# Kernel optimization log

Hardware: AMD Instinct MI355X
Metric: run time of the kernel (lower is better)

Reference implementation:

```python
import jax, jax.numpy as jnp
import numpy as np

NUM_CLASS = 4096
HIDDEN = 512
N_GROUPS = 64  # per branch (co and cl)
BATCH = 64


def _make_group_of(rng, n_groups, num_class):
    # Ragged partition of [0, num_class) into n_groups contiguous segments,
    # mirroring len_co_list_index offsets of the original module.
    cuts = np.sort(rng.choice(np.arange(1, num_class), size=n_groups - 1, replace=False))
    sizes = np.diff(np.concatenate([[0], cuts, [num_class]]))
    return np.repeat(np.arange(n_groups), sizes)  # [num_class] -> group id per class slot


def setup_inputs() -> dict:
    key = jax.random.key(0)
    k_x, k_cow, k_clw, k_cob, k_clb = jax.random.split(key, 5)
    rng = np.random.default_rng(0)
    stdv = 1.0 / np.sqrt(HIDDEN)  # matches reset_parameters uniform(-stdv, stdv)

    x = jax.random.normal(k_x, (BATCH, 2 * N_GROUPS, HIDDEN), dtype=jnp.float32)
    co_W = jax.random.uniform(k_cow, (1, NUM_CLASS, HIDDEN), jnp.float32, -stdv, stdv)
    cl_W = jax.random.uniform(k_clw, (1, NUM_CLASS, HIDDEN), jnp.float32, -stdv, stdv)
    co_b = jax.random.uniform(k_cob, (1, NUM_CLASS), jnp.float32, -stdv, stdv)
    cl_b = jax.random.uniform(k_clb, (1, NUM_CLASS), jnp.float32, -stdv, stdv)

    co_group_of = jnp.asarray(_make_group_of(rng, N_GROUPS, NUM_CLASS), jnp.int32)
    cl_group_of = jnp.asarray(_make_group_of(rng, N_GROUPS, NUM_CLASS), jnp.int32)
    # co_index / cl_index are class-id permutations applied after concat
    co_index = jnp.asarray(rng.permutation(NUM_CLASS), jnp.int32)
    cl_index = jnp.asarray(rng.permutation(NUM_CLASS), jnp.int32)

    return {
        "x": x,
        "co_W": co_W, "cl_W": cl_W,
        "co_b": co_b, "cl_b": cl_b,
        "co_group_of": co_group_of, "cl_group_of": cl_group_of,
        "co_index": co_index, "cl_index": cl_index,
        "group_len": N_GROUPS,
    }


def reference(x, co_W, cl_W, co_b, cl_b, co_group_of, cl_group_of, co_index, cl_index, group_len):
    # x: [B, 2*G, H]; first G group-features feed the co branch, rest the cl branch.
    co_x = x[:, :group_len, :]   # [B, G, H]
    cl_x = x[:, group_len:, :]   # [B, G, H]

    # Fused ragged group-wise broadcast-multiply + reduce:
    # out[b, c] = dot(W[0, c], x[b, group_of[c]]) + b[0, c]
    co_out = jnp.einsum("bch,ch->bc", co_x[:, co_group_of, :], co_W[0]) + co_b  # [B, C]
    cl_out = jnp.einsum("bch,ch->bc", cl_x[:, cl_group_of, :], cl_W[0]) + cl_b  # [B, C]

    # Final index_select gather over classes
    return co_out[:, co_index], cl_out[:, cl_index]
```

## Files before the change

### kernel.cpp

```cpp
#include <hip/hip_runtime.h>
#include <hip/hip_bf16.h>
#include <string.h>

#define NUM_CLASS 4096
#define HIDDEN    512
#define NGROUPS   64
#define BATCH     64

#define WS_NWORK 0
#define WS_WORK  16
#define WS_INV   10240
#define TMP_OFF_F 16384
#define TMP_H_STRIDE (4096*64)
#define TMP_S_STRIDE (2*4096*64)

typedef __attribute__((ext_vector_type(8))) short short8;
typedef __attribute__((ext_vector_type(4))) float f32x4;

__device__ __forceinline__ unsigned int pack2bf(float a, float b) {
    __hip_bfloat16 ha = __float2bfloat16(a), hb = __float2bfloat16(b);
    unsigned short ua, ub;
    memcpy(&ua, &ha, 2); memcpy(&ub, &hb, 2);
    return (unsigned int)ua | ((unsigned int)ub << 16);
}

template<bool WITH_INV>
__global__ __launch_bounds__(1024) void prep_kernel(
    const int* __restrict__ co_gof, const int* __restrict__ cl_gof,
    const int* __restrict__ co_idx, const int* __restrict__ cl_idx,
    int* __restrict__ ws)
{
    __shared__ int s_starts[2][65];
    int tid = threadIdx.x;
    for (int v = tid; v < 2 * NUM_CLASS; v += 1024) {
        int h = v >> 12, c = v & (NUM_CLASS - 1);
        const int* gof = h ? cl_gof : co_gof;
        int g = gof[c];
        if (c == 0) { s_starts[h][0] = 0; s_starts[h][64] = NUM_CLASS; }
        else if (g != gof[c - 1]) s_starts[h][g] = c;
        if (WITH_INV) {
            const int* idx = h ? cl_idx : co_idx;
            ws[WS_INV + h * NUM_CLASS + idx[c]] = c;
        }
    }
    __syncthreads();
    if (tid < 64) {
        int lane = tid;
        for (int h = 0; h < 2; ++h) {
            int s = s_starts[h][lane], e = s_starts[h][lane + 1];
            int cnt = (e - s + 63) >> 6;
            int inc = cnt;
            #pragma unroll
            for (int d = 1; d < 64; d <<= 1) {
                int o = __shfl_up(inc, d, 64);
                if (lane >= d) inc += o;
            }
            int excl = inc - cnt;
            for (int t = 0; t < cnt; ++t) {
                int c0 = s + t * 64;
                int ncls = min(64, e - c0);
                ws[WS_WORK + h * 128 + excl + t] = (lane << 20) | (ncls << 12) | c0;
            }
            if (lane == 63) ws[WS_NWORK + h] = inc;
        }
    }
}

template<int KS, bool SCATTER>
__global__ __launch_bounds__(256, 4) void gwl_stage1(
    const float* __restrict__ x,
    const float* __restrict__ co_W, const float* __restrict__ cl_W,
    const float* __restrict__ co_b, const float* __restrict__ cl_b,
    int* __restrict__ ws, float* __restrict__ out)
{
    const int nblk = 128 * 2 * KS;
    const int chunk = nblk >> 3;
    int bid = blockIdx.x;
    int swz = (bid & 7) * chunk + (bid >> 3);
    int widx = swz & 127;
    int hk   = swz >> 7;
    int h    = hk & 1;
    int kh   = hk >> 1;

    int nw = ws[WS_NWORK + h];
    if (widx >= nw) return;
    int packed = ws[WS_WORK + h * 128 + widx];
    int c0 = packed & 0xFFF, ncls = (packed >> 12) & 0xFF, g = packed >> 20;
    const float* Wp = h ? cl_W : co_W;
    int xrow = h * 64 + g;

    __shared__ __align__(16) unsigned char smem[2][18432];

    int tid = threadIdx.x;
    int l = tid & 63, w = tid >> 6;

    int rowq[4], kvq[4], wcl[4];
    #pragma unroll
    for (int q = 0; q < 4; ++q) {
        int v = q * 256 + tid;
        rowq[q] = v >> 4;
        kvq[q]  = v & 15;
        wcl[q]  = min(rowq[q], ncls - 1);
    }

    float4 rxA[4], rwA[4], rxB[4], rwB[4];
    f32x4 acc[4];
    #pragma unroll
    for (int i = 0; i < 4; ++i) acc[i] = (f32x4)(0.0f);

    const int NCH = 8 / KS;
    const int kbase = kh * (HIDDEN / KS);

#define LOADC(T, RX, RW) do {                                                       \
    int k0_ = kbase + (T) * 64;                                                     \
    _Pragma("unroll")                                                               \
    for (int q = 0; q < 4; ++q) {                                                   \
        RX[q] = *(const float4*)(x + rowq[q] * 65536 + xrow * 512 + k0_ + kvq[q]*4);\
        RW[q] = *(const float4*)(Wp + (c0 + wcl[q]) * 512 + k0_ + kvq[q] * 4);      \
    } } while (0)

#define STOREC(BUF, RX, RW) do {                                                    \
    unsigned short (*Xs_)[72]  = (unsigned short(*)[72])smem[BUF];                  \
    unsigned short (*Wls_)[72] = (unsigned short(*)[72])(smem[BUF] + 9216);         \
    _Pragma("unroll")                                                               \
    for (int q = 0; q < 4; ++q) {                                                   \
        unsigned int x0 = pack2bf(RX[q].x, RX[q].y);                                \
        unsigned int x1 = pack2bf(RX[q].z, RX[q].w);                                \
        unsigned int w0 = pack2bf(RW[q].x, RW[q].y);                                \
        unsigned int w1 = pack2bf(RW[q].z, RW[q].w);                                \
        *(uint2*)&Xs_[rowq[q]][kvq[q] * 4]  = make_uint2(x0, x1);                   \
        *(uint2*)&Wls_[rowq[q]][kvq[q] * 4] = make_uint2(w0, w1);                   \
    } } while (0)

#define COMPUTEC(BUF) do {                                                          \
    unsigned short (*Xs_)[72]  = (unsigned short(*)[72])smem[BUF];                  \
    unsigned short (*Wls_)[72] = (unsigned short(*)[72])(smem[BUF] + 9216);         \
    _Pragma("unroll")                                                               \
    for (int kq = 0; kq < 2; ++kq) {                                                \
        int koff = kq * 32 + (l >> 4) * 8;                                          \
        short8 bfrag = *(const short8*)&Wls_[w * 16 + (l & 15)][koff];              \
        _Pragma("unroll")                                                           \
        for (int i = 0; i < 4; ++i) {                                               \
            short8 afrag = *(const short8*)&Xs_[16 * i + (l & 15)][koff];           \
            acc[i] = __builtin_amdgcn_mfma_f32_16x16x32_bf16(afrag, bfrag, acc[i],  \
                                                             0, 0, 0);              \
        }                                                                           \
    } } while (0)

    LOADC(0, rxA, rwA);
    if (NCH > 1) LOADC(1, rxB, rwB);
    STOREC(0, rxA, rwA);
    __syncthreads();
    #pragma unroll
    for (int t = 0; t < NCH; ++t) {
        if (t + 2 < NCH) {
            if (t & 1) LOADC(t + 2, rxB, rwB);
            else       LOADC(t + 2, rxA, rwA);
        }
        if (t + 1 < NCH) {
            if (t & 1) STOREC((t + 1) & 1, rxA, rwA);
            else       STOREC((t + 1) & 1, rxB, rwB);
        }
        COMPUTEC(t & 1);
        __syncthreads();
    }

    float (*ftile)[65] = (float(*)[65])smem[0];
    #pragma unroll
    for (int i = 0; i < 4; ++i)
        #pragma unroll
        for (int r = 0; r < 4; ++r)
            ftile[w * 16 + (l & 15)][16 * i + (l >> 4) * 4 + r] = acc[i][r];
    __syncthreads();

    if (!SCATTER) {
        float* tmph = (float*)ws + TMP_OFF_F + (size_t)(kh * 2 + h) * TMP_H_STRIDE;
        #pragma unroll
        for (int p = 0; p < 4; ++p) {
            int f = p * 256 + tid;
            int slot = f >> 4, b4 = (f & 15) * 4;
            if (slot < ncls)
                *(float4*)&tmph[(size_t)(c0 + slot) * 64 + b4] =
                    *(const float4*)&ftile[slot][b4];
        }
    } else {
        const float* bias = h ? cl_b : co_b;
        const int*   inv  = ws + WS_INV + h * NUM_CLASS;
        float* outh = out + (size_t)h * BATCH * NUM_CLASS;
        #pragma unroll
        for (int p = 0; p < 4; ++p) {
            int f = p * 256 + tid;
            int slot = f >> 4, b4 = (f & 15) * 4;
            if (slot < ncls) {
                int c = c0 + slot;
                int oc = inv[c];
                float bb = bias[c];
                #pragma unroll
                for (int e = 0; e < 4; ++e)
                    outh[(b4 + e) * 4096 + oc] = ftile[slot][b4 + e] + bb;
            }
        }
    }
#undef LOADC
#undef STOREC
#undef COMPUTEC
}

template<int KS>
__global__ __launch_bounds__(256) void gwl_permute(
    const int* __restrict__ ws,
    const float* __restrict__ co_b, const float* __restrict__ cl_b,
    const int* __restrict__ co_idx, const int* __restrict__ cl_idx,
    float* __restrict__ out)
{
    int jc = blockIdx.x;
    int h  = blockIdx.y;
    const float* bias = h ? cl_b : co_b;
    const int*   idx  = h ? cl_idx : co_idx;
    const float* tmph = (const float*)ws + TMP_OFF_F + (size_t)h * TMP_H_STRIDE;

    __shared__ float tile[64][65];
    int tid = threadIdx.x;
    int lane = tid & 63, w = tid >> 6;

    #pragma unroll
    for (int u = 0; u < 16; ++u) {
        int jj = u * 4 + w;
        int j  = jc * 64 + jj;
        int c  = idx[j];
        float v = bias[c];
        #pragma unroll
        for (int s = 0; s < KS; ++s)
            v += tmph[(size_t)s * TMP_S_STRIDE + (size_t)c * 64 + lane];
        tile[lane][jj] = v;
    }
    __syncthreads();

    #pragma unroll
    for (int p = 0; p < 4; ++p) {
        int f = p * 256 + tid;
        int b = f >> 4, j4 = (f & 15) * 4;
        *(float4*)&out[((size_t)h * 64 + b) * 4096 + jc * 64 + j4] =
            *(const float4*)&tile[b][j4];
    }
}

extern "C" void kernel_launch(void* const* d_in, const int* in_sizes, int n_in,
                              void* d_out, int out_size, void* d_ws, size_t ws_size,
                              hipStream_t stream)
{
    (void)in_sizes; (void)n_in; (void)out_size;
    const float* x      = (const float*)d_in[0];
    const float* co_W   = (const float*)d_in[1];
    const float* cl_W   = (const float*)d_in[2];
    const float* co_b   = (const float*)d_in[3];
    const float* cl_b   = (const float*)d_in[4];
    const int*   co_gof = (const int*)d_in[5];
    const int*   cl_gof = (const int*)d_in[6];
    const int*   co_idx = (const int*)d_in[7];
    const int*   cl_idx = (const int*)d_in[8];
    int*   ws  = (int*)d_ws;
    float* out = (float*)d_out;

    const size_t base  = (size_t)TMP_OFF_F * 4;
    const size_t slice = (size_t)TMP_S_STRIDE * 4;

    if (ws_size >= base + 4 * slice) {
        hipLaunchKernelGGL((prep_kernel<false>), dim3(1), dim3(1024), 0, stream,
                           co_gof, cl_gof, co_idx, cl_idx, ws);
        hipLaunchKernelGGL((gwl_stage1<4, false>), dim3(1024), dim3(256), 0, stream,
                           x, co_W, cl_W, co_b, cl_b, ws, out);
        hipLaunchKernelGGL((gwl_permute<4>), dim3(64, 2), dim3(256), 0, stream,
                           ws, co_b, cl_b, co_idx, cl_idx, out);
    } else if (ws_size >= base + 2 * slice) {
        hipLaunchKernelGGL((prep_kernel<false>), dim3(1), dim3(1024), 0, stream,
                           co_gof, cl_gof, co_idx, cl_idx, ws);
        hipLaunchKernelGGL((gwl_stage1<2, false>), dim3(512), dim3(256), 0, stream,
                           x, co_W, cl_W, co_b, cl_b, ws, out);
        hipLaunchKernelGGL((gwl_permute<2>), dim3(64, 2), dim3(256), 0, stream,
                           ws, co_b, cl_b, co_idx, cl_idx, out);
    } else if (ws_size >= base + 1 * slice) {
        hipLaunchKernelGGL((prep_kernel<false>), dim3(1), dim3(1024), 0, stream,
                           co_gof, cl_gof, co_idx, cl_idx, ws);
        hipLaunchKernelGGL((gwl_stage1<1, false>), dim3(256), dim3(256), 0, stream,
                           x, co_W, cl_W, co_b, cl_b, ws, out);
        hipLaunchKernelGGL((gwl_permute<1>), dim3(64, 2), dim3(256), 0, stream,
                           ws, co_b, cl_b, co_idx, cl_idx, out);
    } else {
        hipLaunchKernelGGL((prep_kernel<true>), dim3(1), dim3(1024), 0, stream,
                           co_gof, cl_gof, co_idx, cl_idx, ws);
        hipLaunchKernelGGL((gwl_stage1<1, true>), dim3(256), dim3(256), 0, stream,
                           x, co_W, cl_W, co_b, cl_b, ws, out);
    }
}
```

Before: 22.97 us.

## Replace prep-kernel work list with fixed 64-class tiles and in-block segment detection

Drops the single-block prep kernel that built a ragged work list. Each stage1 block now owns a fixed 64-class tile and finds group segments itself with a wavefront ballot, then loops over those segments, reloading the x row per segment and flushing the accumulator into a shared tile at each segment boundary. K-split is raised to 8 when the workspace allows it. This removes a serial launch and the workspace round trip, at the cost of extra x loads and MFMA passes for tiles that span several groups, and only a single LDS buffer with extra barriers.

```diff
diff --git a/kernel.cpp b/kernel.cpp
--- a/kernel.cpp
+++ b/kernel.cpp
@@ -7,8 +7,6 @@
 #define NGROUPS   64
 #define BATCH     64
 
-#define WS_NWORK 0
-#define WS_WORK  16
 #define WS_INV   10240
 #define TMP_OFF_F 16384
 #define TMP_H_STRIDE (4096*64)
@@ -24,45 +22,15 @@
     return (unsigned int)ua | ((unsigned int)ub << 16);
 }
 
-template<bool WITH_INV>
-__global__ __launch_bounds__(1024) void prep_kernel(
-    const int* __restrict__ co_gof, const int* __restrict__ cl_gof,
+__global__ __launch_bounds__(1024) void prep_inv_kernel(
     const int* __restrict__ co_idx, const int* __restrict__ cl_idx,
     int* __restrict__ ws)
 {
-    __shared__ int s_starts[2][65];
     int tid = threadIdx.x;
     for (int v = tid; v < 2 * NUM_CLASS; v += 1024) {
         int h = v >> 12, c = v & (NUM_CLASS - 1);
-        const int* gof = h ? cl_gof : co_gof;
-        int g = gof[c];
-        if (c == 0) { s_starts[h][0] = 0; s_starts[h][64] = NUM_CLASS; }
-        else if (g != gof[c - 1]) s_starts[h][g] = c;
-        if (WITH_INV) {
-            const int* idx = h ? cl_idx : co_idx;
-            ws[WS_INV + h * NUM_CLASS + idx[c]] = c;
-        }
-    }
-    __syncthreads();
-    if (tid < 64) {
-        int lane = tid;
-        for (int h = 0; h < 2; ++h) {
-            int s = s_starts[h][lane], e = s_starts[h][lane + 1];
-            int cnt = (e - s + 63) >> 6;
-            int inc = cnt;
-            #pragma unroll
-            for (int d = 1; d < 64; d <<= 1) {
-                int o = __shfl_up(inc, d, 64);
-                if (lane >= d) inc += o;
-            }
-            int excl = inc - cnt;
-            for (int t = 0; t < cnt; ++t) {
-                int c0 = s + t * 64;
-                int ncls = min(64, e - c0);
-                ws[WS_WORK + h * 128 + excl + t] = (lane << 20) | (ncls << 12) | c0;
-            }
-            if (lane == 63) ws[WS_NWORK + h] = inc;
-        }
+        const int* idx = h ? cl_idx : co_idx;
+        ws[WS_INV + h * NUM_CLASS + idx[c]] = c;
     }
 }
 
@@ -71,36 +39,53 @@
     const float* __restrict__ x,
     const float* __restrict__ co_W, const float* __restrict__ cl_W,
     const float* __restrict__ co_b, const float* __restrict__ cl_b,
+    const int* __restrict__ co_gof, const int* __restrict__ cl_gof,
     int* __restrict__ ws, float* __restrict__ out)
 {
-    const int nblk = 128 * 2 * KS;
+    const int NCH = 8 / KS;
+    const int nblk = 128 * KS;
     const int chunk = nblk >> 3;
     int bid = blockIdx.x;
     int swz = (bid & 7) * chunk + (bid >> 3);
-    int widx = swz & 127;
-    int hk   = swz >> 7;
-    int h    = hk & 1;
-    int kh   = hk >> 1;
-
-    int nw = ws[WS_NWORK + h];
-    if (widx >= nw) return;
-    int packed = ws[WS_WORK + h * 128 + widx];
-    int c0 = packed & 0xFFF, ncls = (packed >> 12) & 0xFF, g = packed >> 20;
-    const float* Wp = h ? cl_W : co_W;
-    int xrow = h * 64 + g;
-
-    __shared__ __align__(16) unsigned char smem[2][18432];
+    int cid = swz & 63;
+    int hk  = swz >> 6;
+    int h   = hk & 1;
+    int kh  = hk >> 1;
+    int c0  = cid * 64;
+
+    const float* Wp  = h ? cl_W : co_W;
+    const int*   gof = h ? cl_gof : co_gof;
+
+    __shared__ __align__(16) unsigned short Xs[64][72];
+    __shared__ __align__(16) unsigned short Wls[64][72];
+    __shared__ float ftile[64][65];
+    __shared__ int s_seg_lo[65];
+    __shared__ int s_seg_g[64];
+    __shared__ int s_nseg;
 
     int tid = threadIdx.x;
     int l = tid & 63, w = tid >> 6;
 
-    int rowq[4], kvq[4], wcl[4];
+    if (tid < 64) {
+        int gi = gof[c0 + tid];
+        int prev = (tid == 0) ? -1 : gof[c0 + tid - 1];
+        bool is_start = (gi != prev);
+        unsigned long long m = __ballot(is_start);
+        int segidx = (int)__popcll(m & ((1ull << tid) - 1ull));
+        if (is_start) { s_seg_lo[segidx] = tid; s_seg_g[segidx] = gi; }
+        if (tid == 0) {
+            int ns = (int)__popcll(m);
+            s_nseg = ns;
+            s_seg_lo[ns] = 64;
+        }
+    }
+
+    int rowq[4], kvq[4];
     #pragma unroll
     for (int q = 0; q < 4; ++q) {
         int v = q * 256 + tid;
         rowq[q] = v >> 4;
         kvq[q]  = v & 15;
-        wcl[q]  = min(rowq[q], ncls - 1);
     }
 
     float4 rxA[4], rwA[4], rxB[4], rwB[4];
@@ -108,70 +93,83 @@
     #pragma unroll
     for (int i = 0; i < 4; ++i) acc[i] = (f32x4)(0.0f);
 
-    const int NCH = 8 / KS;
     const int kbase = kh * (HIDDEN / KS);
 
-#define LOADC(T, RX, RW) do {                                                       \
-    int k0_ = kbase + (T) * 64;                                                     \
+#define LOADC(S, RX, RW, NEEDW) do {                                                \
+    int si_ = (S) / NCH, t_ = (S) % NCH;                                            \
+    int k0_ = kbase + t_ * 64;                                                      \
+    int xr_ = h * 64 + s_seg_g[si_];                                                \
     _Pragma("unroll")                                                               \
     for (int q = 0; q < 4; ++q) {                                                   \
-        RX[q] = *(const float4*)(x + rowq[q] * 65536 + xrow * 512 + k0_ + kvq[q]*4);\
-        RW[q] = *(const float4*)(Wp + (c0 + wcl[q]) * 512 + k0_ + kvq[q] * 4);      \
+        RX[q] = *(const float4*)(x + rowq[q] * 65536 + xr_ * 512 + k0_ + kvq[q]*4); \
+        if (NEEDW)                                                                  \
+            RW[q] = *(const float4*)(Wp + (c0 + rowq[q]) * 512 + k0_ + kvq[q] * 4); \
     } } while (0)
 
-#define STOREC(BUF, RX, RW) do {                                                    \
-    unsigned short (*Xs_)[72]  = (unsigned short(*)[72])smem[BUF];                  \
-    unsigned short (*Wls_)[72] = (unsigned short(*)[72])(smem[BUF] + 9216);         \
+#define STOREC(RX, RW, NEEDW) do {                                                  \
     _Pragma("unroll")                                                               \
     for (int q = 0; q < 4; ++q) {                                                   \
         unsigned int x0 = pack2bf(RX[q].x, RX[q].y);                                \
         unsigned int x1 = pack2bf(RX[q].z, RX[q].w);                                \
-        unsigned int w0 = pack2bf(RW[q].x, RW[q].y);                                \
-        unsigned int w1 = pack2bf(RW[q].z, RW[q].w);                                \
-        *(uint2*)&Xs_[rowq[q]][kvq[q] * 4]  = make_uint2(x0, x1);                   \
-        *(uint2*)&Wls_[rowq[q]][kvq[q] * 4] = make_uint2(w0, w1);                   \
+        *(uint2*)&Xs[rowq[q]][kvq[q] * 4] = make_uint2(x0, x1);                     \
+        if (NEEDW) {                                                                \
+            unsigned int w0 = pack2bf(RW[q].x, RW[q].y);                            \
+            unsigned int w1 = pack2bf(RW[q].z, RW[q].w);                            \
+            *(uint2*)&Wls[rowq[q]][kvq[q] * 4] = make_uint2(w0, w1);                \
+        }                                                                           \
     } } while (0)
 
-#define COMPUTEC(BUF) do {                                                          \
-    unsigned short (*Xs_)[72]  = (unsigned short(*)[72])smem[BUF];                  \
-    unsigned short (*Wls_)[72] = (unsigned short(*)[72])(smem[BUF] + 9216);         \
+#define COMPUTEC() do {                                                             \
     _Pragma("unroll")                                                               \
     for (int kq = 0; kq < 2; ++kq) {                                                \
         int koff = kq * 32 + (l >> 4) * 8;                                          \
-        short8 bfrag = *(const short8*)&Wls_[w * 16 + (l & 15)][koff];              \
+        short8 bfrag = *(const short8*)&Wls[w * 16 + (l & 15)][koff];               \
         _Pragma("unroll")                                                           \
         for (int i = 0; i < 4; ++i) {                                               \
-            short8 afrag = *(const short8*)&Xs_[16 * i + (l & 15)][koff];           \
+            short8 afrag = *(const short8*)&Xs[16 * i + (l & 15)][koff];            \
             acc[i] = __builtin_amdgcn_mfma_f32_16x16x32_bf16(afrag, bfrag, acc[i],  \
                                                              0, 0, 0);              \
         }                                                                           \
     } } while (0)
 
-    LOADC(0, rxA, rwA);
-    if (NCH > 1) LOADC(1, rxB, rwB);
-    STOREC(0, rxA, rwA);
     __syncthreads();
-    #pragma unroll
-    for (int t = 0; t < NCH; ++t) {
-        if (t + 2 < NCH) {
-            if (t & 1) LOADC(t + 2, rxB, rwB);
-            else       LOADC(t + 2, rxA, rwA);
-        }
-        if (t + 1 < NCH) {
-            if (t & 1) STOREC((t + 1) & 1, rxA, rwA);
-            else       STOREC((t + 1) & 1, rxB, rwB);
-        }
-        COMPUTEC(t & 1);
+    int nseg = s_nseg;
+    int nsteps = nseg * NCH;
+    int slotw = w * 16 + (l & 15);
+
+    LOADC(0, rxA, rwA, true);
+    STOREC(rxA, rwA, true);
+    __syncthreads();
+
+    #pragma unroll 1
+    for (int s = 0; s < nsteps; ++s) {
+        bool nxt = (s + 1 < nsteps);
+        const bool needW = (NCH > 1);
+        if (nxt) {
+            if (s & 1) LOADC(s + 1, rxA, rwA, needW);
+            else       LOADC(s + 1, rxB, rwB, needW);
+        }
+        COMPUTEC();
+        if ((s % NCH) == NCH - 1) {
+            int si = s / NCH;
+            int lo = s_seg_lo[si], hi = s_seg_lo[si + 1];
+            if (slotw >= lo && slotw < hi) {
+                #pragma unroll
+                for (int i = 0; i < 4; ++i)
+                    #pragma unroll
+                    for (int r = 0; r < 4; ++r)
+                        ftile[slotw][16 * i + (l >> 4) * 4 + r] = acc[i][r];
+            }
+            #pragma unroll
+            for (int i = 0; i < 4; ++i) acc[i] = (f32x4)(0.0f);
+        }
         __syncthreads();
-    }
-
-    float (*ftile)[65] = (float(*)[65])smem[0];
-    #pragma unroll
-    for (int i = 0; i < 4; ++i)
-        #pragma unroll
-        for (int r = 0; r < 4; ++r)
-            ftile[w * 16 + (l & 15)][16 * i + (l >> 4) * 4 + r] = acc[i][r];
-    __syncthreads();
+        if (nxt) {
+            if (s & 1) STOREC(rxA, rwA, needW);
+            else       STOREC(rxB, rwB, needW);
+            __syncthreads();
+        }
+    }
 
     if (!SCATTER) {
         float* tmph = (float*)ws + TMP_OFF_F + (size_t)(kh * 2 + h) * TMP_H_STRIDE;
@@ -179,9 +177,8 @@
         for (int p = 0; p < 4; ++p) {
             int f = p * 256 + tid;
             int slot = f >> 4, b4 = (f & 15) * 4;
-            if (slot < ncls)
-                *(float4*)&tmph[(size_t)(c0 + slot) * 64 + b4] =
-                    *(const float4*)&ftile[slot][b4];
+            *(float4*)&tmph[(size_t)(c0 + slot) * 64 + b4] =
+                *(const float4*)&ftile[slot][b4];
         }
     } else {
         const float* bias = h ? cl_b : co_b;
@@ -191,14 +188,12 @@
         for (int p = 0; p < 4; ++p) {
             int f = p * 256 + tid;
             int slot = f >> 4, b4 = (f & 15) * 4;
-            if (slot < ncls) {
-                int c = c0 + slot;
-                int oc = inv[c];
-                float bb = bias[c];
-                #pragma unroll
-                for (int e = 0; e < 4; ++e)
-                    outh[(b4 + e) * 4096 + oc] = ftile[slot][b4 + e] + bb;
-            }
+            int c = c0 + slot;
+            int oc = inv[c];
+            float bb = bias[c];
+            #pragma unroll
+            for (int e = 0; e < 4; ++e)
+                outh[(b4 + e) * 4096 + oc] = ftile[slot][b4 + e] + bb;
         }
     }
 #undef LOADC
@@ -265,31 +260,30 @@
     const size_t base  = (size_t)TMP_OFF_F * 4;
     const size_t slice = (size_t)TMP_S_STRIDE * 4;
 
-    if (ws_size >= base + 4 * slice) {
-        hipLaunchKernelGGL((prep_kernel<false>), dim3(1), dim3(1024), 0, stream,
-                           co_gof, cl_gof, co_idx, cl_idx, ws);
-        hipLaunchKernelGGL((gwl_stage1<4, false>), dim3(1024), dim3(256), 0, stream,
-                           x, co_W, cl_W, co_b, cl_b, ws, out);
+    if (ws_size >= base + 8 * slice) {
+        hipLaunchKernelGGL((gwl_stage1<8, false>), dim3(1024), dim3(256), 0, stream,
+                           x, co_W, cl_W, co_b, cl_b, co_gof, cl_gof, ws, out);
+        hipLaunchKernelGGL((gwl_permute<8>), dim3(64, 2), dim3(256), 0, stream,
+                           ws, co_b, cl_b, co_idx, cl_idx, out);
+    } else if (ws_size >= base + 4 * slice) {
+        hipLaunchKernelGGL((gwl_stage1<4, false>), dim3(512), dim3(256), 0, stream,
+                           x, co_W, cl_W, co_b, cl_b, co_gof, cl_gof, ws, out);
         hipLaunchKernelGGL((gwl_permute<4>), dim3(64, 2), dim3(256), 0, stream,
                            ws, co_b, cl_b, co_idx, cl_idx, out);
     } else if (ws_size >= base + 2 * slice) {
-        hipLaunchKernelGGL((prep_kernel<false>), dim3(1), dim3(1024), 0, stream,
-                           co_gof, cl_gof, co_idx, cl_idx, ws);
-        hipLaunchKernelGGL((gwl_stage1<2, false>), dim3(512), dim3(256), 0, stream,
-                           x, co_W, cl_W, co_b, cl_b, ws, out);
+        hipLaunchKernelGGL((gwl_stage1<2, false>), dim3(256), dim3(256), 0, stream,
+                           x, co_W, cl_W, co_b, cl_b, co_gof, cl_gof, ws, out);
         hipLaunchKernelGGL((gwl_permute<2>), dim3(64, 2), dim3(256), 0, stream,
                            ws, co_b, cl_b, co_idx, cl_idx, out);
     } else if (ws_size >= base + 1 * slice) {
-        hipLaunchKernelGGL((prep_kernel<false>), dim3(1), dim3(1024), 0, stream,
-                           co_gof, cl_gof, co_idx, cl_idx, ws);
-        hipLaunchKernelGGL((gwl_stage1<1, false>), dim3(256), dim3(256), 0, stream,
-                           x, co_W, cl_W, co_b, cl_b, ws, out);
+        hipLaunchKernelGGL((gwl_stage1<1, false>), dim3(128), dim3(256), 0, stream,
+                           x, co_W, cl_W, co_b, cl_b, co_gof, cl_gof, ws, out);
         hipLaunchKernelGGL((gwl_permute<1>), dim3(64, 2), dim3(256), 0, stream,
                            ws, co_b, cl_b, co_idx, cl_idx, out);
     } else {
-        hipLaunchKernelGGL((prep_kernel<true>), dim3(1), dim3(1024), 0, stream,
-                           co_gof, cl_gof, co_idx, cl_idx, ws);
-        hipLaunchKernelGGL((gwl_stage1<1, true>), dim3(256), dim3(256), 0, stream,
-                           x, co_W, cl_W, co_b, cl_b, ws, out);
-    }
-}
+        hipLaunchKernelGGL(prep_inv_kernel, dim3(1), dim3(1024), 0, stream,
+                           co_idx, cl_idx, ws);
+        hipLaunchKernelGGL((gwl_stage1<1, true>), dim3(128), dim3(256), 0, stream,
+                           x, co_W, cl_W, co_b, cl_b, co_gof, cl_gof, ws, out);
+    }
+}
```

Result: no change. 23.32 us (+1.5%).
